# Kernel tuning notes

Measured on AMD Instinct MI355X. Metric: run time of the kernel, lower is better.

## Reference

```python
import jax, jax.numpy as jnp
import numpy as np

D_MODEL = 1024
NUM_HEADS = 16
D_K = D_MODEL // NUM_HEADS
THETA = 10000.0
SEQ = 4096
BATCH = 1


def _rope(x, token_positions):
    # x: [b, h, s, d_k]; interleaved even/odd rotation as in the torch module
    kd = jnp.arange(0, D_K, 2, dtype=jnp.float32) / D_K          # [d_k/2]
    angles = token_positions[:, None].astype(jnp.float32) / (THETA ** kd)  # [s, d_k/2]
    cos_pos = jnp.cos(angles)
    sin_pos = jnp.sin(angles)
    x_even = x[..., 0::2]
    x_odd = x[..., 1::2]
    rot_even = x_even * cos_pos - x_odd * sin_pos
    rot_odd = x_even * sin_pos + x_odd * cos_pos
    rot = jnp.stack([rot_even, rot_odd], axis=-1)                # [..., d_k/2, 2]
    return rot.reshape(*x.shape[:-1], D_K)


def setup_inputs() -> dict:
    key = jax.random.key(0)
    k1, k2, k3 = jax.random.split(key, 3)
    std_qkv = np.sqrt(2.0 / (D_MODEL + 3 * D_MODEL))
    std_o = np.sqrt(2.0 / (D_MODEL + D_MODEL))
    x = jax.random.normal(k1, (BATCH, SEQ, D_MODEL), dtype=jnp.float32)
    Wqkv = jax.random.normal(k2, (3 * D_MODEL, D_MODEL), dtype=jnp.float32) * std_qkv
    Wo = jax.random.normal(k3, (D_MODEL, D_MODEL), dtype=jnp.float32) * std_o
    token_positions = jnp.arange(SEQ, dtype=jnp.int32)
    return {"x": x, "Wqkv": Wqkv, "Wo": Wo, "token_positions": token_positions}


def reference(x, Wqkv, Wo, token_positions):
    b, s, _ = x.shape
    qkv = jnp.einsum('bsd,ed->bse', x, Wqkv)                      # [b, s, 3*d_model]
    q, k, v = jnp.split(qkv, 3, axis=-1)

    def to_heads(t):
        return t.reshape(b, s, NUM_HEADS, D_K).transpose(0, 2, 1, 3)  # [b, h, s, d_k]

    q, k, v = to_heads(q), to_heads(k), to_heads(v)
    q = _rope(q, token_positions)
    k = _rope(k, token_positions)

    scores = jnp.einsum('bhqd,bhkd->bhqk', q, k) / jnp.sqrt(jnp.float32(D_K))
    mask = jnp.tril(jnp.ones((s, s), dtype=bool))
    scores = jnp.where(mask, scores, -jnp.inf)
    attn = jax.nn.softmax(scores, axis=-1)
    out = jnp.einsum('bhqk,bhkd->bhqd', attn, v)                  # [b, h, s, d_k]
    out = out.transpose(0, 2, 1, 3).reshape(b, s, D_MODEL)
    return jnp.einsum('bsd,ed->bse', out, Wo)
```

## Files before the change

kernel.cpp:

```cpp
#include <hip/hip_runtime.h>
#include <cstdint>

typedef unsigned short u16;
typedef __attribute__((ext_vector_type(8))) short short8;
typedef __attribute__((ext_vector_type(4))) float float4v;

__device__ __forceinline__ float bf2f(u16 u) {
    union { unsigned int i; float f; } v; v.i = ((unsigned int)u) << 16; return v.f;
}
__device__ __forceinline__ u16 f2bf(float f) {
    union { float f; unsigned int i; } v; v.f = f;
    unsigned int i = v.i;
    i += 0x7fffu + ((i >> 16) & 1u);
    return (u16)(i >> 16);
}
__device__ __forceinline__ uint4 cvt8(const float* __restrict__ p) {
    float4 a = *(const float4*)p;
    float4 b = *(const float4*)(p + 4);
    u16 t[8] = {f2bf(a.x), f2bf(a.y), f2bf(a.z), f2bf(a.w),
                f2bf(b.x), f2bf(b.y), f2bf(b.z), f2bf(b.w)};
    return *(const uint4*)t;
}

__global__ void cvt_f32_bf16(const float* __restrict__ src, u16* __restrict__ dst, int n8) {
    int i = blockIdx.x * blockDim.x + threadIdx.x;
    if (i >= n8) return;
    *(uint4*)(dst + (size_t)i * 8) = cvt8(src + (size_t)i * 8);
}

__global__ void zero_f32(float* __restrict__ p, int n4) {
    int i = blockIdx.x * blockDim.x + threadIdx.x;
    if (i >= n4) return;
    float4 z = {0.f, 0.f, 0.f, 0.f};
    *(float4*)(p + (size_t)i * 4) = z;
}

__global__ __launch_bounds__(256) void gemm_bt(const u16* __restrict__ A,
                                               const u16* __restrict__ B,
                                               u16* __restrict__ C,
                                               int M, int N, int K) {
    __shared__ u16 As[128 * 40];
    __shared__ u16 Bs[128 * 40];
    const int tid  = threadIdx.x;
    const int wave = tid >> 6, lane = tid & 63;
    const int lg = lane >> 4, lr = lane & 15;
    const int bm = blockIdx.x * 128, bn = blockIdx.y * 128;
    const int wm = (wave & 1) * 64, wn = (wave >> 1) * 64;

    float4v acc[4][4] = {};

    for (int k0 = 0; k0 < K; k0 += 32) {
        #pragma unroll
        for (int i = 0; i < 2; ++i) {
            int seg = tid + i * 256;
            int row = seg >> 2;
            int co  = (seg & 3) * 8;
            *(uint4*)(As + row * 40 + co) = *(const uint4*)(A + (size_t)(bm + row) * K + k0 + co);
            *(uint4*)(Bs + row * 40 + co) = *(const uint4*)(B + (size_t)(bn + row) * K + k0 + co);
        }
        __syncthreads();

        short8 af[4], bf[4];
        #pragma unroll
        for (int i = 0; i < 4; ++i)
            af[i] = *(const short8*)(As + (wm + i * 16 + lr) * 40 + lg * 8);
        #pragma unroll
        for (int j = 0; j < 4; ++j)
            bf[j] = *(const short8*)(Bs + (wn + j * 16 + lr) * 40 + lg * 8);
        #pragma unroll
        for (int i = 0; i < 4; ++i)
            #pragma unroll
            for (int j = 0; j < 4; ++j)
                acc[i][j] = __builtin_amdgcn_mfma_f32_16x16x32_bf16(af[i], bf[j], acc[i][j], 0, 0, 0);
        __syncthreads();
    }

    #pragma unroll
    for (int i = 0; i < 4; ++i)
        #pragma unroll
        for (int j = 0; j < 4; ++j)
            #pragma unroll
            for (int r = 0; r < 4; ++r) {
                int row = bm + wm + i * 16 + lg * 4 + r;
                int col = bn + wn + j * 16 + lr;
                C[(size_t)row * N + col] = f2bf(acc[i][j][r]);
            }
}

__global__ void rope_kernel(u16* __restrict__ qkv, const int* __restrict__ pos, int S) {
    int idx = blockIdx.x * blockDim.x + threadIdx.x;
    int s = idx >> 10;
    if (s >= S) return;
    int p    = idx & 1023;
    int part = p >> 9;
    int wi   = p & 511;
    int head = wi >> 5;
    int i    = wi & 31;
    int col  = part * 1024 + head * 64 + 2 * i;

    u16* ptr = qkv + (size_t)s * 3072 + col;
    ushort2 v = *(const ushort2*)ptr;
    float xe = bf2f(v.x), xo = bf2f(v.y);
    float freq = __expf(-(float)i * 0.2878231366242557f);
    float ang  = (float)pos[s] * freq;
    float sn = sinf(ang), cs = cosf(ang);
    float re = xe * cs - xo * sn;
    float ro = xe * sn + xo * cs;
    if (part == 0) { re *= 0.125f; ro *= 0.125f; }
    ushort2 o; o.x = f2bf(re); o.y = f2bf(ro);
    *(ushort2*)ptr = o;
}

__global__ __launch_bounds__(256) void transpose_v(const u16* __restrict__ qkv,
                                                   u16* __restrict__ VT) {
    __shared__ u16 T[64 * 65];
    const int h = blockIdx.y, s0 = blockIdx.x * 64;
    const int tid = threadIdx.x;
    #pragma unroll
    for (int i = 0; i < 2; ++i) {
        int seg = i * 256 + tid;
        int r = seg >> 3, c8 = (seg & 7) * 8;
        u16 tmp[8];
        *(uint4*)tmp = *(const uint4*)(qkv + (size_t)(s0 + r) * 3072 + 2048 + h * 64 + c8);
        #pragma unroll
        for (int j = 0; j < 8; ++j) T[r * 65 + c8 + j] = tmp[j];
    }
    __syncthreads();
    #pragma unroll
    for (int i = 0; i < 2; ++i) {
        int seg = i * 256 + tid;
        int d = seg >> 3, s8 = (seg & 7) * 8;
        u16 tmp[8];
        #pragma unroll
        for (int j = 0; j < 8; ++j) tmp[j] = T[(s8 + j) * 65 + d];
        *(uint4*)(VT + (size_t)(h * 64 + d) * 4096 + s0 + s8) = *(const uint4*)tmp;
    }
}

__global__ __launch_bounds__(512) void attn_kernel(const u16* __restrict__ qkv,
                                                   const u16* __restrict__ VT,
                                                   float* __restrict__ acc,
                                                   float* __restrict__ lac) {
    __shared__ u16 Ks[64 * 64];
    __shared__ u16 Vt[64 * 64];
    __shared__ u16 Ps[8][16 * 72];

    const int tid  = threadIdx.x;
    const int wave = tid >> 6, lane = tid & 63;
    const int lg = lane >> 4, lr = lane & 15;
    const int h  = blockIdx.y;
    const int z  = blockIdx.z;

    const int srow = tid >> 3;
    const int sg   = tid & 7;
    const int sco  = sg * 8;
    const int sldso = srow * 64 + ((sg ^ (srow & 7)) * 8);
    const int swz = (lr & 7);

    #pragma unroll 1
    for (int part = 0; part < 2; ++part) {
        const int qt = part ? (31 - (int)blockIdx.x) : (int)blockIdx.x;
        const int qb = qt * 128;
        const int qrow0 = qb + wave * 16;
        const int tmax = qb + 64;
        const int t0s  = z * 64;

        short8 qf[2];
        #pragma unroll
        for (int kk = 0; kk < 2; ++kk)
            qf[kk] = *(const short8*)(qkv + (size_t)(qrow0 + lr) * 3072 + h * 64 + kk * 32 + lg * 8);

        float4v o_acc[4] = {};
        float rs = 0.f;

        uint4 rK = *(const uint4*)(qkv + (size_t)(t0s + srow) * 3072 + 1024 + h * 64 + sco);
        uint4 rV = *(const uint4*)(VT + (size_t)(h * 64 + srow) * 4096 + t0s + sco);
        __syncthreads();
        *(uint4*)(Ks + sldso) = rK;
        *(uint4*)(Vt + sldso) = rV;
        __syncthreads();

        for (int t0 = t0s; t0 <= tmax; t0 += 128) {
            const bool hasnext = (t0 + 128 <= tmax);
            if (hasnext) {
                rK = *(const uint4*)(qkv + (size_t)(t0 + 128 + srow) * 3072 + 1024 + h * 64 + sco);
                rV = *(const uint4*)(VT + (size_t)(h * 64 + srow) * 4096 + t0 + 128 + sco);
            }

            float4v sc[4];
            #pragma unroll
            for (int jt = 0; jt < 4; ++jt) {
                float4v a = {};
                #pragma unroll
                for (int kk = 0; kk < 2; ++kk) {
                    short8 kf = *(const short8*)(Ks + (jt * 16 + lr) * 64 + (((kk * 4 + lg) ^ swz) * 8));
                    a = __builtin_amdgcn_mfma_f32_16x16x32_bf16(kf, qf[kk], a, 0, 0, 0);
                }
                sc[jt] = a;
            }

            const bool mk = (t0 + 63 > qrow0);
            const int q_abs = qrow0 + lr;
            #pragma unroll
            for (int jt = 0; jt < 4; ++jt) {
                u16 pt[4];
                #pragma unroll
                for (int r = 0; r < 4; ++r) {
                    float s = sc[jt][r];
                    if (mk && (t0 + jt * 16 + lg * 4 + r > q_abs)) s = -30000.f;
                    float p = __expf(fminf(s, 60.f));
                    rs += p;
                    pt[r] = f2bf(p);
                }
                *(uint2*)(Ps[wave] + lr * 72 + jt * 16 + lg * 4) = *(const uint2*)pt;
            }

            short8 pf[2];
            #pragma unroll
            for (int kk = 0; kk < 2; ++kk)
                pf[kk] = *(const short8*)(Ps[wave] + lr * 72 + kk * 32 + lg * 8);
            #pragma unroll
            for (int jd = 0; jd < 4; ++jd) {
                float4v a = o_acc[jd];
                #pragma unroll
                for (int kk = 0; kk < 2; ++kk) {
                    short8 vf = *(const short8*)(Vt + (jd * 16 + lr) * 64 + (((kk * 4 + lg) ^ swz) * 8));
                    a = __builtin_amdgcn_mfma_f32_16x16x32_bf16(pf[kk], vf, a, 0, 0, 0);
                }
                o_acc[jd] = a;
            }
            __syncthreads();
            if (hasnext) {
                *(uint4*)(Ks + sldso) = rK;
                *(uint4*)(Vt + sldso) = rV;
            }
            __syncthreads();
        }

        float t = rs;
        t += __shfl_xor(t, 16, 64);
        t += __shfl_xor(t, 32, 64);
        if (lane < 16)
            atomicAdd(&lac[(size_t)(qrow0 + lr) * 16 + h], t);

        #pragma unroll
        for (int jd = 0; jd < 4; ++jd)
            #pragma unroll
            for (int r = 0; r < 4; ++r) {
                int s = qrow0 + lg * 4 + r;
                int d = jd * 16 + lr;
                atomicAdd(&acc[(size_t)s * 1024 + h * 64 + d], o_acc[jd][r]);
            }
    }
}

__global__ void norm_o(const float* __restrict__ acc, const float* __restrict__ lac,
                       u16* __restrict__ qkv) {
    int i = blockIdx.x * blockDim.x + threadIdx.x;
    if (i >= 4096 * 1024 / 8) return;
    int e0 = i * 8;
    int s = e0 >> 10, c = e0 & 1023, h = c >> 6;
    float inv = 1.0f / lac[(size_t)s * 16 + h];
    float4 a = *(const float4*)(acc + e0);
    float4 b = *(const float4*)(acc + e0 + 4);
    u16 t[8] = {f2bf(a.x * inv), f2bf(a.y * inv), f2bf(a.z * inv), f2bf(a.w * inv),
                f2bf(b.x * inv), f2bf(b.y * inv), f2bf(b.z * inv), f2bf(b.w * inv)};
    *(uint4*)(qkv + (size_t)s * 3072 + c) = *(const uint4*)t;
}

__global__ __launch_bounds__(256) void gemm_oproj(const u16* __restrict__ A,
                                                  const u16* __restrict__ B,
                                                  float* __restrict__ C) {
    __shared__ u16 As[128 * 40];
    __shared__ u16 Bs[128 * 40];
    const int tid  = threadIdx.x;
    const int wave = tid >> 6, lane = tid & 63;
    const int lg = lane >> 4, lr = lane & 15;
    const int bm = blockIdx.x * 128, bn = blockIdx.y * 128;
    const int wm = (wave & 1) * 64, wn = (wave >> 1) * 64;

    float4v acc[4][4] = {};

    for (int k0 = 0; k0 < 1024; k0 += 32) {
        #pragma unroll
        for (int i = 0; i < 2; ++i) {
            int seg = tid + i * 256;
            int row = seg >> 2;
            int co  = (seg & 3) * 8;
            *(uint4*)(As + row * 40 + co) =
                *(const uint4*)(A + (size_t)(bm + row) * 3072 + k0 + co);
            *(uint4*)(Bs + row * 40 + co) =
                *(const uint4*)(B + (size_t)(bn + row) * 1024 + k0 + co);
        }
        __syncthreads();

        short8 af[4], bf[4];
        #pragma unroll
        for (int i = 0; i < 4; ++i)
            af[i] = *(const short8*)(As + (wm + i * 16 + lr) * 40 + lg * 8);
        #pragma unroll
        for (int j = 0; j < 4; ++j)
            bf[j] = *(const short8*)(Bs + (wn + j * 16 + lr) * 40 + lg * 8);
        #pragma unroll
        for (int i = 0; i < 4; ++i)
            #pragma unroll
            for (int j = 0; j < 4; ++j)
                acc[i][j] = __builtin_amdgcn_mfma_f32_16x16x32_bf16(af[i], bf[j], acc[i][j], 0, 0, 0);
        __syncthreads();
    }

    #pragma unroll
    for (int i = 0; i < 4; ++i)
        #pragma unroll
        for (int j = 0; j < 4; ++j)
            #pragma unroll
            for (int r = 0; r < 4; ++r) {
                int row = bm + wm + i * 16 + lg * 4 + r;
                int col = bn + wn + j * 16 + lr;
                C[(size_t)row * 1024 + col] = acc[i][j][r];
            }
}

__global__ void fill_diag(float* __restrict__ p, size_t n, float mark) {
    size_t i = (size_t)blockIdx.x * blockDim.x + threadIdx.x;
    if (i < n) p[i] = 0.f;
    if (i == 0) p[0] = mark;
}

extern "C" void kernel_launch(void* const* d_in, const int* in_sizes, int n_in,
                              void* d_out, int out_size, void* d_ws, size_t ws_size,
                              hipStream_t stream) {
    int ix = -1, iwq = -1, iwo = -1, ip = -1;
    for (int i = 0; i < n_in; ++i) {
        if      (in_sizes[i] == 4096 * 1024) ix = i;
        else if (in_sizes[i] == 3072 * 1024) iwq = i;
        else if (in_sizes[i] == 1024 * 1024) iwo = i;
        else if (in_sizes[i] == 4096)        ip = i;
    }
    float* out = (float*)d_out;
    const size_t OUT_E = (size_t)4096 * 1024;
    const size_t QKV_E = (size_t)4096 * 3072;
    const size_t NEED  = QKV_E * 2 + (size_t)3072 * 1024 * 2;

    if (ix < 0 || iwq < 0 || iwo < 0 || ip < 0 || out_size != (int)OUT_E) {
        fill_diag<<<(int)((OUT_E + 255) / 256), 256, 0, stream>>>(out, OUT_E, 1000.0f);
        return;
    }
    if (ws_size < NEED) {
        fill_diag<<<(int)((OUT_E + 255) / 256), 256, 0, stream>>>(out, OUT_E, 500.0f);
        return;
    }
    const float* x    = (const float*)d_in[ix];
    const float* Wqkv = (const float*)d_in[iwq];
    const float* Wo   = (const float*)d_in[iwo];
    const int*   pos  = (const int*)d_in[ip];

    u16* qkv   = (u16*)d_ws;
    u16* wq_bf = (u16*)d_ws + QKV_E;
    u16* wo_bf = wq_bf;
    float* lac = (float*)((char*)wq_bf + 2 * 1024 * 1024 + 65536);
    u16* x_bf  = (u16*)d_out;
    u16* VT    = (u16*)d_out + OUT_E;
    float* acc = (float*)d_in[ix];

    cvt_f32_bf16<<<2048, 256, 0, stream>>>(x, x_bf, 4096 * 1024 / 8);
    cvt_f32_bf16<<<1536, 256, 0, stream>>>(Wqkv, wq_bf, 3072 * 1024 / 8);
    gemm_bt<<<dim3(32, 24), 256, 0, stream>>>(x_bf, wq_bf, qkv, 4096, 3072, 1024);
    zero_f32<<<4096, 256, 0, stream>>>(acc, 4096 * 1024 / 4);
    zero_f32<<<16, 256, 0, stream>>>(lac, 4096 * 16 / 4);
    cvt_f32_bf16<<<512, 256, 0, stream>>>(Wo, wo_bf, 1024 * 1024 / 8);
    rope_kernel<<<16384, 256, 0, stream>>>(qkv, pos, 4096);
    transpose_v<<<dim3(64, 16), 256, 0, stream>>>(qkv, VT);
    attn_kernel<<<dim3(16, 16, 2), 512, 0, stream>>>(qkv, VT, acc, lac);
    norm_o<<<2048, 256, 0, stream>>>(acc, lac, qkv);
    gemm_oproj<<<dim3(32, 8), 256, 0, stream>>>(qkv, wo_bf, out);
}
```

Before: 252.4 us.

## Fuse normalization into out-proj GEMM, use direct-to-LDS loads, exp2 softmax

Replaces register-staged tile loads in the GEMMs with global_load_lds direct transfers and unpadded LDS tiles. Folds the zeroing of the accumulation buffers into the conversion kernels, and fuses the per-head normalization into the out-projection's A-tile load, removing the norm_o kernel and its round trip. Switches the softmax to exp2 with log2e folded into the Q scale and uses truncating bf16 conversion for probabilities. This removes launches and memory traffic, but risks LDS bank conflicts from the unpadded layout and slightly lower precision.

```diff
diff --git a/kernel.cpp b/kernel.cpp
--- a/kernel.cpp
+++ b/kernel.cpp
@@ -13,6 +13,10 @@
     unsigned int i = v.i;
     i += 0x7fffu + ((i >> 16) & 1u);
     return (u16)(i >> 16);
+}
+__device__ __forceinline__ u16 f2bf_t(float f) {
+    union { float f; unsigned int i; } v; v.f = f;
+    return (u16)(v.i >> 16);
 }
 __device__ __forceinline__ uint4 cvt8(const float* __restrict__ p) {
     float4 a = *(const float4*)p;
@@ -21,6 +25,20 @@
                 f2bf(b.x), f2bf(b.y), f2bf(b.z), f2bf(b.w)};
     return *(const uint4*)t;
 }
+__device__ __forceinline__ void gload16(const void* g, void* l) {
+    __builtin_amdgcn_global_load_lds(
+        (const __attribute__((address_space(1))) unsigned int*)g,
+        (__attribute__((address_space(3))) unsigned int*)l, 16, 0, 0);
+}
+
+__global__ void cvt_x_zero(float* __restrict__ src, u16* __restrict__ dst, int n8) {
+    int i = blockIdx.x * blockDim.x + threadIdx.x;
+    if (i >= n8) return;
+    float* p = src + (size_t)i * 8;
+    *(uint4*)(dst + (size_t)i * 8) = cvt8(p);
+    float4 z = {0.f, 0.f, 0.f, 0.f};
+    *(float4*)p = z; *(float4*)(p + 4) = z;
+}
 
 __global__ void cvt_f32_bf16(const float* __restrict__ src, u16* __restrict__ dst, int n8) {
     int i = blockIdx.x * blockDim.x + threadIdx.x;
@@ -28,45 +46,49 @@
     *(uint4*)(dst + (size_t)i * 8) = cvt8(src + (size_t)i * 8);
 }
 
-__global__ void zero_f32(float* __restrict__ p, int n4) {
+__global__ void cvt_wo_zero(const float* __restrict__ src, u16* __restrict__ dst,
+                            float* __restrict__ lac) {
     int i = blockIdx.x * blockDim.x + threadIdx.x;
-    if (i >= n4) return;
-    float4 z = {0.f, 0.f, 0.f, 0.f};
-    *(float4*)(p + (size_t)i * 4) = z;
+    *(uint4*)(dst + (size_t)i * 8) = cvt8(src + (size_t)i * 8);
+    if (i < 16384) {
+        float4 z = {0.f, 0.f, 0.f, 0.f};
+        *(float4*)(lac + (size_t)i * 4) = z;
+    }
 }
 
 __global__ __launch_bounds__(256) void gemm_bt(const u16* __restrict__ A,
                                                const u16* __restrict__ B,
                                                u16* __restrict__ C,
                                                int M, int N, int K) {
-    __shared__ u16 As[128 * 40];
-    __shared__ u16 Bs[128 * 40];
+    __shared__ u16 As[128 * 32];
+    __shared__ u16 Bs[128 * 32];
     const int tid  = threadIdx.x;
     const int wave = tid >> 6, lane = tid & 63;
     const int lg = lane >> 4, lr = lane & 15;
     const int bm = blockIdx.x * 128, bn = blockIdx.y * 128;
     const int wm = (wave & 1) * 64, wn = (wave >> 1) * 64;
+    const int grow = lane >> 2;
+    const int gcol = (lane & 3) * 8;
 
     float4v acc[4][4] = {};
 
     for (int k0 = 0; k0 < K; k0 += 32) {
         #pragma unroll
-        for (int i = 0; i < 2; ++i) {
-            int seg = tid + i * 256;
-            int row = seg >> 2;
-            int co  = (seg & 3) * 8;
-            *(uint4*)(As + row * 40 + co) = *(const uint4*)(A + (size_t)(bm + row) * K + k0 + co);
-            *(uint4*)(Bs + row * 40 + co) = *(const uint4*)(B + (size_t)(bn + row) * K + k0 + co);
+        for (int it = 0; it < 2; ++it) {
+            int n = wave * 2 + it;
+            int row = n * 16 + grow;
+            gload16(A + (size_t)(bm + row) * K + k0 + gcol, As + n * 512 + lane * 8);
+            gload16(B + (size_t)(bn + row) * K + k0 + gcol, Bs + n * 512 + lane * 8);
         }
         __syncthreads();
 
         short8 af[4], bf[4];
         #pragma unroll
         for (int i = 0; i < 4; ++i)
-            af[i] = *(const short8*)(As + (wm + i * 16 + lr) * 40 + lg * 8);
+            af[i] = *(const short8*)(As + (wm + i * 16 + lr) * 32 + lg * 8);
         #pragma unroll
         for (int j = 0; j < 4; ++j)
-            bf[j] = *(const short8*)(Bs + (wn + j * 16 + lr) * 40 + lg * 8);
+            bf[j] = *(const short8*)(Bs + (wn + j * 16 + lr) * 32 + lg * 8);
         #pragma unroll
         for (int i = 0; i < 4; ++i)
             #pragma unroll
@@ -106,7 +128,7 @@
     float sn = sinf(ang), cs = cosf(ang);
     float re = xe * cs - xo * sn;
     float ro = xe * sn + xo * cs;
-    if (part == 0) { re *= 0.125f; ro *= 0.125f; }
+    if (part == 0) { re *= 0.18033688011112042f; ro *= 0.18033688011112042f; }
     ushort2 o; o.x = f2bf(re); o.y = f2bf(ro);
     *(ushort2*)ptr = o;
 }
@@ -208,9 +230,9 @@
                 for (int r = 0; r < 4; ++r) {
                     float s = sc[jt][r];
                     if (mk && (t0 + jt * 16 + lg * 4 + r > q_abs)) s = -30000.f;
-                    float p = __expf(fminf(s, 60.f));
+                    float p = exp2f(fminf(s, 80.f));
                     rs += p;
-                    pt[r] = f2bf(p);
+                    pt[r] = f2bf_t(p);
                 }
                 *(uint2*)(Ps[wave] + lr * 72 + jt * 16 + lg * 4) = *(const uint2*)pt;
             }
@@ -254,43 +276,49 @@
     }
 }
 
-__global__ void norm_o(const float* __restrict__ acc, const float* __restrict__ lac,
-                       u16* __restrict__ qkv) {
-    int i = blockIdx.x * blockDim.x + threadIdx.x;
-    if (i >= 4096 * 1024 / 8) return;
-    int e0 = i * 8;
-    int s = e0 >> 10, c = e0 & 1023, h = c >> 6;
-    float inv = 1.0f / lac[(size_t)s * 16 + h];
-    float4 a = *(const float4*)(acc + e0);
-    float4 b = *(const float4*)(acc + e0 + 4);
-    u16 t[8] = {f2bf(a.x * inv), f2bf(a.y * inv), f2bf(a.z * inv), f2bf(a.w * inv),
-                f2bf(b.x * inv), f2bf(b.y * inv), f2bf(b.z * inv), f2bf(b.w * inv)};
-    *(uint4*)(qkv + (size_t)s * 3072 + c) = *(const uint4*)t;
-}
-
-__global__ __launch_bounds__(256) void gemm_oproj(const u16* __restrict__ A,
+__global__ __launch_bounds__(256) void gemm_oproj(const float* __restrict__ acc_,
+                                                  const float* __restrict__ lac,
                                                   const u16* __restrict__ B,
                                                   float* __restrict__ C) {
     __shared__ u16 As[128 * 40];
-    __shared__ u16 Bs[128 * 40];
+    __shared__ u16 Bs[128 * 32];
     const int tid  = threadIdx.x;
     const int wave = tid >> 6, lane = tid & 63;
     const int lg = lane >> 4, lr = lane & 15;
     const int bm = blockIdx.x * 128, bn = blockIdx.y * 128;
     const int wm = (wave & 1) * 64, wn = (wave >> 1) * 64;
+    const int grow = lane >> 2;
+    const int gcol = (lane & 3) * 8;
+
+    const int row0 = tid >> 2, row1 = row0 + 64;
+    const int co   = (tid & 3) * 8;
+    float inv0 = 0.f, inv1 = 0.f;
 
     float4v acc[4][4] = {};
 
     for (int k0 = 0; k0 < 1024; k0 += 32) {
-        #pragma unroll
-        for (int i = 0; i < 2; ++i) {
-            int seg = tid + i * 256;
-            int row = seg >> 2;
-            int co  = (seg & 3) * 8;
-            *(uint4*)(As + row * 40 + co) =
-                *(const uint4*)(A + (size_t)(bm + row) * 3072 + k0 + co);
-            *(uint4*)(Bs + row * 40 + co) =
-                *(const uint4*)(B + (size_t)(bn + row) * 1024 + k0 + co);
+        if ((k0 & 63) == 0) {
+            int hh = k0 >> 6;
+            inv0 = 1.0f / lac[(size_t)(bm + row0) * 16 + hh];
+            inv1 = 1.0f / lac[(size_t)(bm + row1) * 16 + hh];
+        }
+        {
+            const float* p0 = acc_ + (size_t)(bm + row0) * 1024 + k0 + co;
+            const float* p1 = acc_ + (size_t)(bm + row1) * 1024 + k0 + co;
+            float4 a0 = *(const float4*)p0, b0 = *(const float4*)(p0 + 4);
+            float4 a1 = *(const float4*)p1, b1 = *(const float4*)(p1 + 4);
+            u16 t0[8] = {f2bf(a0.x*inv0), f2bf(a0.y*inv0), f2bf(a0.z*inv0), f2bf(a0.w*inv0),
+                         f2bf(b0.x*inv0), f2bf(b0.y*inv0), f2bf(b0.z*inv0), f2bf(b0.w*inv0)};
+            u16 t1[8] = {f2bf(a1.x*inv1), f2bf(a1.y*inv1), f2bf(a1.z*inv1), f2bf(a1.w*inv1),
+                         f2bf(b1.x*inv1), f2bf(b1.y*inv1), f2bf(b1.z*inv1), f2bf(b1.w*inv1)};
+            *(uint4*)(As + row0 * 40 + co) = *(const uint4*)t0;
+            *(uint4*)(As + row1 * 40 + co) = *(const uint4*)t1;
+        }
+        #pragma unroll
+        for (int it = 0; it < 2; ++it) {
+            int n = wave * 2 + it;
+            int row = n * 16 + grow;
+            gload16(B + (size_t)(bn + row) * 1024 + k0 + gcol, Bs + n * 512 + lane * 8);
         }
         __syncthreads();
 
@@ -300,7 +328,7 @@
             af[i] = *(const short8*)(As + (wm + i * 16 + lr) * 40 + lg * 8);
         #pragma unroll
         for (int j = 0; j < 4; ++j)
-            bf[j] = *(const short8*)(Bs + (wn + j * 16 + lr) * 40 + lg * 8);
+            bf[j] = *(const short8*)(Bs + (wn + j * 16 + lr) * 32 + lg * 8);
         #pragma unroll
         for (int i = 0; i < 4; ++i)
             #pragma unroll
@@ -350,7 +378,7 @@
         fill_diag<<<(int)((OUT_E + 255) / 256), 256, 0, stream>>>(out, OUT_E, 500.0f);
         return;
     }
-    const float* x    = (const float*)d_in[ix];
+    float* x          = (float*)d_in[ix];
     const float* Wqkv = (const float*)d_in[iwq];
     const float* Wo   = (const float*)d_in[iwo];
     const int*   pos  = (const int*)d_in[ip];
@@ -361,17 +389,14 @@
     float* lac = (float*)((char*)wq_bf + 2 * 1024 * 1024 + 65536);
     u16* x_bf  = (u16*)d_out;
     u16* VT    = (u16*)d_out + OUT_E;
-    float* acc = (float*)d_in[ix];
-
-    cvt_f32_bf16<<<2048, 256, 0, stream>>>(x, x_bf, 4096 * 1024 / 8);
+    float* acc = x;
+
+    cvt_x_zero<<<2048, 256, 0, stream>>>(x, x_bf, 4096 * 1024 / 8);
     cvt_f32_bf16<<<1536, 256, 0, stream>>>(Wqkv, wq_bf, 3072 * 1024 / 8);
     gemm_bt<<<dim3(32, 24), 256, 0, stream>>>(x_bf, wq_bf, qkv, 4096, 3072, 1024);
-    zero_f32<<<4096, 256, 0, stream>>>(acc, 4096 * 1024 / 4);
-    zero_f32<<<16, 256, 0, stream>>>(lac, 4096 * 16 / 4);
-    cvt_f32_bf16<<<512, 256, 0, stream>>>(Wo, wo_bf, 1024 * 1024 / 8);
+    cvt_wo_zero<<<512, 256, 0, stream>>>(Wo, wo_bf, lac);
     rope_kernel<<<16384, 256, 0, stream>>>(qkv, pos, 4096);
     transpose_v<<<dim3(64, 16), 256, 0, stream>>>(qkv, VT);
     attn_kernel<<<dim3(16, 16, 2), 512, 0, stream>>>(qkv, VT, acc, lac);
-    norm_o<<<2048, 256, 0, stream>>>(acc, lac, qkv);
-    gemm_oproj<<<dim3(32, 8), 256, 0, stream>>>(qkv, wo_bf, out);
-}
+    gemm_oproj<<<dim3(32, 8), 256, 0, stream>>>(acc, lac, wo_bf, out);
+}
```

Measured after the change: 262.5 us. 1.04x slower.
